# Kernel optimization log

Hardware: AMD Instinct MI355X
Metric: run time of the kernel (lower is better)

## Reference

```python
import jax, jax.numpy as jnp
import numpy as np

NG, NC, FG, FC, D = 8192, 4096, 512, 256, 64
ALPHA = 0.2          # leaky_relu negative slope
NEG = -9.0e15        # mask fill value from the torch code


def _leaky(x):
    return jnp.where(x >= 0, x, ALPHA * x)


def _relation(h_src, h_dst, a, adj):
    # additive GAT score: e[i,j] = leaky(h_src[i]@a[:D] + h_dst[j]@a[D:])
    s1 = h_src @ a[:D]            # [Ns]
    s2 = h_dst @ a[D:]            # [Nd]
    e = _leaky(s1[:, None] + s2[None, :])          # [Ns, Nd]
    att = jax.nn.softmax(jnp.where(adj > 0, e, NEG), axis=1)
    return att @ h_dst            # [Ns, D]


def setup_inputs() -> dict:
    key = jax.random.key(0)
    ks = jax.random.split(key, 14)
    sc = 0.05
    return {
        "gene_x": jax.random.normal(ks[0], (NG, FG), jnp.float32),
        "cell_x": jax.random.normal(ks[1], (NC, FC), jnp.float32),
        "W_g": jax.random.normal(ks[2], (FG, D), jnp.float32) * sc,
        "W_c": jax.random.normal(ks[3], (FC, D), jnp.float32) * sc,
        "a_gg": jax.random.normal(ks[4], (2 * D,), jnp.float32) * sc,
        "a_gc": jax.random.normal(ks[5], (2 * D,), jnp.float32) * sc,
        "a_cc": jax.random.normal(ks[6], (2 * D,), jnp.float32) * sc,
        "a_cg": jax.random.normal(ks[7], (2 * D,), jnp.float32) * sc,
        "Wgate_g": jax.random.normal(ks[8], (D, 1), jnp.float32) * sc,
        "bgate_g": jnp.full((1,), -2.0, jnp.float32),
        "Wgate_c": jax.random.normal(ks[9], (D, 1), jnp.float32) * sc,
        "bgate_c": jnp.full((1,), -2.0, jnp.float32),
        "gene_adj": jax.random.randint(ks[10], (NG, NG), 0, 2, jnp.int32),
        "cell_adj": jax.random.randint(ks[11], (NC, NC), 0, 2, jnp.int32),
        "gene_cell_adj": jax.random.randint(ks[12], (NG, NC), 0, 2, jnp.int32),
    }


def reference(gene_x, cell_x, W_g, W_c, a_gg, a_gc, a_cc, a_cg,
              Wgate_g, bgate_g, Wgate_c, bgate_c,
              gene_adj, cell_adj, gene_cell_adj):
    gene_h = gene_x @ W_g                              # [NG, D]
    cell_h = cell_x @ W_c                              # [NC, D]

    gene_from_gene = _relation(gene_h, gene_h, a_gg, gene_adj)
    gene_from_cell = _relation(gene_h, cell_h, a_gc, gene_cell_adj)
    cell_from_cell = _relation(cell_h, cell_h, a_cc, cell_adj)
    cell_from_gene = _relation(cell_h, gene_h, a_cg, gene_cell_adj.T)

    gamma_g = jax.nn.sigmoid(gene_h @ Wgate_g + bgate_g)   # [NG, 1]
    gamma_c = jax.nn.sigmoid(cell_h @ Wgate_c + bgate_c)   # [NC, 1]

    gene_out = _leaky(gene_h + gene_from_gene + gamma_g * gene_from_cell)
    cell_out = _leaky(cell_h + cell_from_cell + gamma_c * cell_from_gene)
    return gene_out, cell_out
```

## Files before the change

### kernel.cpp

```cpp
#include <hip/hip_runtime.h>

#define NG 8192
#define NC 4096
#define FG 512
#define FC 256
#define ALPHA 0.2f

typedef float f32x4 __attribute__((ext_vector_type(4)));
typedef short bf16x8 __attribute__((ext_vector_type(8)));

static __device__ __forceinline__ float leakyf(float x) { return fmaxf(x, ALPHA * x); }

static __device__ __forceinline__ unsigned short f2bf(float f) {
    unsigned u = __builtin_bit_cast(unsigned, f);
    u += 0x7fffu + ((u >> 16) & 1u);
    return (unsigned short)(u >> 16);
}

static __device__ __forceinline__ float wred(float v) {
#pragma unroll
    for (int m = 1; m < 64; m <<= 1) v += __shfl_xor(v, m, 64);
    return v;
}

__global__ __launch_bounds__(256) void proj_kernel(
    const float* __restrict__ x, const float* __restrict__ W, int K, int N,
    float* __restrict__ h, unsigned short* __restrict__ hT,
    const float* __restrict__ aA, const float* __restrict__ aB,
    const float* __restrict__ aC, const float* __restrict__ aD,
    const float* __restrict__ aG, const float* __restrict__ bG,
    float* __restrict__ sA, float* __restrict__ sB, float* __restrict__ sC,
    float* __restrict__ sD, float* __restrict__ gam)
{
    const int wave = threadIdx.x >> 6, lane = threadIdx.x & 63;
    const int r0 = blockIdx.x * 16 + wave * 4;
    const float* xr = x + (size_t)r0 * K;
    float acc0 = 0.f, acc1 = 0.f, acc2 = 0.f, acc3 = 0.f;
    for (int k = 0; k < K; k += 4) {
        float4 x0 = *(const float4*)(xr + k);
        float4 x1 = *(const float4*)(xr + K + k);
        float4 x2 = *(const float4*)(xr + 2 * (size_t)K + k);
        float4 x3 = *(const float4*)(xr + 3 * (size_t)K + k);
        float w0 = W[(k + 0) * 64 + lane];
        float w1 = W[(k + 1) * 64 + lane];
        float w2 = W[(k + 2) * 64 + lane];
        float w3 = W[(k + 3) * 64 + lane];
        acc0 += x0.x * w0 + x0.y * w1 + x0.z * w2 + x0.w * w3;
        acc1 += x1.x * w0 + x1.y * w1 + x1.z * w2 + x1.w * w3;
        acc2 += x2.x * w0 + x2.y * w1 + x2.z * w2 + x2.w * w3;
        acc3 += x3.x * w0 + x3.y * w1 + x3.z * w2 + x3.w * w3;
    }
    float accs[4] = {acc0, acc1, acc2, acc3};
    unsigned short hb[4];
#pragma unroll
    for (int t = 0; t < 4; t++) {
        h[(size_t)(r0 + t) * 64 + lane] = accs[t];
        hb[t] = f2bf(accs[t]);
    }
    *(ushort4*)&hT[(size_t)lane * N + r0] = make_ushort4(hb[0], hb[1], hb[2], hb[3]);

    const float cA = aA[lane], cB = aB[lane], cC = aC[lane], cD = aD[lane], cG = aG[lane];
    const float bias = bG[0];
#pragma unroll
    for (int t = 0; t < 4; t++) {
        float vA = wred(accs[t] * cA);
        float vB = wred(accs[t] * cB);
        float vC = wred(accs[t] * cC);
        float vD = wred(accs[t] * cD);
        float vG = wred(accs[t] * cG);
        if (lane == 0) {
            sA[r0 + t] = vA; sB[r0 + t] = vB; sC[r0 + t] = vC; sD[r0 + t] = vD;
            gam[r0 + t] = 1.f / (1.f + __expf(-(vG + bias)));
        }
    }
}

__global__ __launch_bounds__(256, 4) void rel_kernel(
    const int* __restrict__ adj, int adj_ld, int transposed,
    const float* __restrict__ s1, const float* __restrict__ s2,
    const unsigned short* __restrict__ hT, int Nd,
    float* __restrict__ num, float* __restrict__ lsum, int Ns, int JS)
{
    __shared__ unsigned short lds[64 * 264];
    const int wave = threadIdx.x >> 6, lane = threadIdx.x & 63;
    const int m = lane & 15, kp = lane >> 4;
    const int strip = blockIdx.x, p = blockIdx.y;
    const int jlen = Nd / JS;
    const int jbase = p * jlen;
    const int i_row = strip * 64 + wave * 16 + m;
    const float s1v = s1[i_row];
    f32x4 acc0 = {0.f, 0.f, 0.f, 0.f}, acc1 = acc0, acc2 = acc0, acc3 = acc0;
    float lacc = 0.f;

    for (int j0 = jbase; j0 < jbase + jlen; j0 += 256) {
        for (int idx = threadIdx.x; idx < 2048; idx += 256) {
            int c = idx >> 5, off = (idx & 31) * 8;
            *(int4*)&lds[c * 264 + off] = *(const int4*)&hT[(size_t)c * Nd + j0 + off];
        }
        __syncthreads();
#pragma unroll
        for (int kk = 0; kk < 8; kk++) {
            const int jg = j0 + kk * 32 + kp * 8;
            float s2v[8];
            {
                float4 sa = *(const float4*)&s2[jg];
                float4 sb = *(const float4*)&s2[jg + 4];
                s2v[0] = sa.x; s2v[1] = sa.y; s2v[2] = sa.z; s2v[3] = sa.w;
                s2v[4] = sb.x; s2v[5] = sb.y; s2v[6] = sb.z; s2v[7] = sb.w;
            }
            int am[8];
            if (!transposed) {
                const int* ar = adj + (size_t)i_row * adj_ld + jg;
                int4 a0 = *(const int4*)ar;
                int4 a1 = *(const int4*)(ar + 4);
                am[0] = a0.x; am[1] = a0.y; am[2] = a0.z; am[3] = a0.w;
                am[4] = a1.x; am[5] = a1.y; am[6] = a1.z; am[7] = a1.w;
            } else {
                const int* ac = adj + (size_t)jg * adj_ld + i_row;
#pragma unroll
                for (int t = 0; t < 8; t++) am[t] = ac[(size_t)t * adj_ld];
            }
            bf16x8 af;
#pragma unroll
            for (int t = 0; t < 8; t++) {
                float e = s1v + s2v[t];
                float w = (am[t] > 0) ? __expf(leakyf(e)) : 0.f;
                lacc += w;
                af[t] = (short)f2bf(w);
            }
            const int lb = kk * 32 + kp * 8;
            bf16x8 b0 = *(const bf16x8*)&lds[(0 * 16 + m) * 264 + lb];
            bf16x8 b1 = *(const bf16x8*)&lds[(1 * 16 + m) * 264 + lb];
            bf16x8 b2 = *(const bf16x8*)&lds[(2 * 16 + m) * 264 + lb];
            bf16x8 b3 = *(const bf16x8*)&lds[(3 * 16 + m) * 264 + lb];
            acc0 = __builtin_amdgcn_mfma_f32_16x16x32_bf16(af, b0, acc0, 0, 0, 0);
            acc1 = __builtin_amdgcn_mfma_f32_16x16x32_bf16(af, b1, acc1, 0, 0, 0);
            acc2 = __builtin_amdgcn_mfma_f32_16x16x32_bf16(af, b2, acc2, 0, 0, 0);
            acc3 = __builtin_amdgcn_mfma_f32_16x16x32_bf16(af, b3, acc3, 0, 0, 0);
        }
        __syncthreads();
    }
    const int orow0 = strip * 64 + wave * 16 + kp * 4;
#pragma unroll
    for (int r = 0; r < 4; r++) {
        size_t base = ((size_t)p * Ns + orow0 + r) * 64;
        num[base + m]      = acc0[r];
        num[base + 16 + m] = acc1[r];
        num[base + 32 + m] = acc2[r];
        num[base + 48 + m] = acc3[r];
    }
    lacc += __shfl_xor(lacc, 16, 64);
    lacc += __shfl_xor(lacc, 32, 64);
    if (kp == 0) lsum[(size_t)p * Ns + strip * 64 + wave * 16 + m] = lacc;
}

__global__ __launch_bounds__(256) void combine_final(
    const float* __restrict__ numS, const float* __restrict__ lS, int JSS,
    const float* __restrict__ numX, const float* __restrict__ lX, int JSX,
    int Ns, const float* __restrict__ h, const float* __restrict__ gam,
    float* __restrict__ out)
{
    int idx = blockIdx.x * 256 + threadIdx.x;
    int i = idx >> 6, c = idx & 63;
    float nS = 0.f, dS = 0.f, nX = 0.f, dX = 0.f;
    for (int p = 0; p < JSS; p++) {
        nS += numS[((size_t)p * Ns + i) * 64 + c];
        dS += lS[(size_t)p * Ns + i];
    }
    for (int p = 0; p < JSX; p++) {
        nX += numX[((size_t)p * Ns + i) * 64 + c];
        dX += lX[(size_t)p * Ns + i];
    }
    float v = h[idx] + nS / dS + gam[i] * (nX / dX);
    out[idx] = leakyf(v);
}

extern "C" void kernel_launch(void* const* d_in, const int* in_sizes, int n_in,
                              void* d_out, int out_size, void* d_ws, size_t ws_size,
                              hipStream_t stream)
{
    const float* gene_x = (const float*)d_in[0];
    const float* cell_x = (const float*)d_in[1];
    const float* W_g    = (const float*)d_in[2];
    const float* W_c    = (const float*)d_in[3];
    const float* a_gg   = (const float*)d_in[4];
    const float* a_gc   = (const float*)d_in[5];
    const float* a_cc   = (const float*)d_in[6];
    const float* a_cg   = (const float*)d_in[7];
    const float* Wgg    = (const float*)d_in[8];
    const float* bgg    = (const float*)d_in[9];
    const float* Wgc    = (const float*)d_in[10];
    const float* bgc    = (const float*)d_in[11];
    const int* gene_adj = (const int*)d_in[12];
    const int* cell_adj = (const int*)d_in[13];
    const int* gc_adj   = (const int*)d_in[14];

    size_t off = 0;
    char* wsb = (char*)d_ws;
    auto alloc = [&](size_t bytes) -> void* {
        void* p = wsb + off;
        off += (bytes + 255) & ~(size_t)255;
        return p;
    };
    const int JS = 16;
    float* gene_h = (float*)alloc((size_t)NG * 64 * 4);
    float* cell_h = (float*)alloc((size_t)NC * 64 * 4);
    unsigned short* gene_hT = (unsigned short*)alloc((size_t)NG * 64 * 2);
    unsigned short* cell_hT = (unsigned short*)alloc((size_t)NC * 64 * 2);
    float* s1gg = (float*)alloc(NG * 4);
    float* s2gg = (float*)alloc(NG * 4);
    float* s1gc = (float*)alloc(NG * 4);
    float* s2cg = (float*)alloc(NG * 4);
    float* gamg = (float*)alloc(NG * 4);
    float* s1cc = (float*)alloc(NC * 4);
    float* s2cc = (float*)alloc(NC * 4);
    float* s2gc = (float*)alloc(NC * 4);
    float* s1cg = (float*)alloc(NC * 4);
    float* gamc = (float*)alloc(NC * 4);
    float* numGG = (float*)alloc((size_t)NG * 64 * JS * 4);
    float* lGG   = (float*)alloc((size_t)NG * JS * 4);
    float* numGC = (float*)alloc((size_t)NG * 64 * JS * 4);
    float* lGC   = (float*)alloc((size_t)NG * JS * 4);
    float* numCC = (float*)alloc((size_t)NC * 64 * JS * 4);
    float* lCC   = (float*)alloc((size_t)NC * JS * 4);
    float* numCG = (float*)alloc((size_t)NC * 64 * JS * 4);
    float* lCG   = (float*)alloc((size_t)NC * JS * 4);

    float* out_gene = (float*)d_out;
    float* out_cell = (float*)d_out + (size_t)NG * 64;

    proj_kernel<<<NG / 16, 256, 0, stream>>>(gene_x, W_g, FG, NG, gene_h, gene_hT,
        a_gg, a_gg + 64, a_gc, a_cg + 64, Wgg, bgg, s1gg, s2gg, s1gc, s2cg, gamg);
    proj_kernel<<<NC / 16, 256, 0, stream>>>(cell_x, W_c, FC, NC, cell_h, cell_hT,
        a_cc, a_cc + 64, a_gc + 64, a_cg, Wgc, bgc, s1cc, s2cc, s2gc, s1cg, gamc);

    rel_kernel<<<dim3(NG / 64, JS), 256, 0, stream>>>(gene_adj, NG, 0, s1gg, s2gg,
        gene_hT, NG, numGG, lGG, NG, JS);
    rel_kernel<<<dim3(NC / 64, JS), 256, 0, stream>>>(cell_adj, NC, 0, s1cc, s2cc,
        cell_hT, NC, numCC, lCC, NC, JS);
    rel_kernel<<<dim3(NG / 64, JS), 256, 0, stream>>>(gc_adj, NC, 0, s1gc, s2gc,
        cell_hT, NC, numGC, lGC, NG, JS);
    rel_kernel<<<dim3(NC / 64, JS), 256, 0, stream>>>(gc_adj, NC, 1, s1cg, s2cg,
        gene_hT, NG, numCG, lCG, NC, JS);

    combine_final<<<NG * 64 / 256, 256, 0, stream>>>(numGG, lGG, JS, numGC, lGC, JS,
        NG, gene_h, gamg, out_gene);
    combine_final<<<NC * 64 / 256, 256, 0, stream>>>(numCC, lCC, JS, numCG, lCG, JS,
        NC, cell_h, gamc, out_cell);
}
```

Measured before the change: 729.4 us.

## Load B operand directly from global memory and retune split factors per relation

Drops the LDS staging of the transposed bf16 features and the block-wide barriers. Each lane now reads its MFMA B fragments straight from global memory, relying on cache hits, and the loop runs over 32-column groups with unroll 2. The column-split factor is cut to 8 for the gene-row relations, which halves partial-sum traffic for those relations but gives fewer blocks. The risk is more redundant global and L2 reads, since the four waves now each fetch the same B data.

```diff
diff --git a/kernel.cpp b/kernel.cpp
--- a/kernel.cpp
+++ b/kernel.cpp
@@ -81,64 +81,56 @@
     const unsigned short* __restrict__ hT, int Nd,
     float* __restrict__ num, float* __restrict__ lsum, int Ns, int JS)
 {
-    __shared__ unsigned short lds[64 * 264];
     const int wave = threadIdx.x >> 6, lane = threadIdx.x & 63;
     const int m = lane & 15, kp = lane >> 4;
     const int strip = blockIdx.x, p = blockIdx.y;
-    const int jlen = Nd / JS;
-    const int jbase = p * jlen;
+    const int jlen = Nd / JS, jbase = p * jlen;
     const int i_row = strip * 64 + wave * 16 + m;
     const float s1v = s1[i_row];
     f32x4 acc0 = {0.f, 0.f, 0.f, 0.f}, acc1 = acc0, acc2 = acc0, acc3 = acc0;
     float lacc = 0.f;
 
-    for (int j0 = jbase; j0 < jbase + jlen; j0 += 256) {
-        for (int idx = threadIdx.x; idx < 2048; idx += 256) {
-            int c = idx >> 5, off = (idx & 31) * 8;
-            *(int4*)&lds[c * 264 + off] = *(const int4*)&hT[(size_t)c * Nd + j0 + off];
+    const unsigned short* hb0 = hT + (size_t)(0 * 16 + m) * Nd;
+    const unsigned short* hb1 = hT + (size_t)(1 * 16 + m) * Nd;
+    const unsigned short* hb2 = hT + (size_t)(2 * 16 + m) * Nd;
+    const unsigned short* hb3 = hT + (size_t)(3 * 16 + m) * Nd;
+
+    const int NGRP = jlen >> 5;
+#pragma unroll 2
+    for (int g = 0; g < NGRP; ++g) {
+        const int jg = jbase + g * 32 + kp * 8;
+        float4 sa = *(const float4*)&s2[jg];
+        float4 sb = *(const float4*)&s2[jg + 4];
+        int am[8];
+        if (!transposed) {
+            const int* ar = adj + (size_t)i_row * adj_ld + jg;
+            int4 a0 = *(const int4*)ar;
+            int4 a1 = *(const int4*)(ar + 4);
+            am[0] = a0.x; am[1] = a0.y; am[2] = a0.z; am[3] = a0.w;
+            am[4] = a1.x; am[5] = a1.y; am[6] = a1.z; am[7] = a1.w;
+        } else {
+            const int* ac = adj + (size_t)jg * adj_ld + i_row;
+#pragma unroll
+            for (int t = 0; t < 8; t++) am[t] = ac[(size_t)t * adj_ld];
         }
-        __syncthreads();
-#pragma unroll
-        for (int kk = 0; kk < 8; kk++) {
-            const int jg = j0 + kk * 32 + kp * 8;
-            float s2v[8];
-            {
-                float4 sa = *(const float4*)&s2[jg];
-                float4 sb = *(const float4*)&s2[jg + 4];
-                s2v[0] = sa.x; s2v[1] = sa.y; s2v[2] = sa.z; s2v[3] = sa.w;
-                s2v[4] = sb.x; s2v[5] = sb.y; s2v[6] = sb.z; s2v[7] = sb.w;
-            }
-            int am[8];
-            if (!transposed) {
-                const int* ar = adj + (size_t)i_row * adj_ld + jg;
-                int4 a0 = *(const int4*)ar;
-                int4 a1 = *(const int4*)(ar + 4);
-                am[0] = a0.x; am[1] = a0.y; am[2] = a0.z; am[3] = a0.w;
-                am[4] = a1.x; am[5] = a1.y; am[6] = a1.z; am[7] = a1.w;
-            } else {
-                const int* ac = adj + (size_t)jg * adj_ld + i_row;
-#pragma unroll
-                for (int t = 0; t < 8; t++) am[t] = ac[(size_t)t * adj_ld];
-            }
-            bf16x8 af;
-#pragma unroll
-            for (int t = 0; t < 8; t++) {
-                float e = s1v + s2v[t];
-                float w = (am[t] > 0) ? __expf(leakyf(e)) : 0.f;
-                lacc += w;
-                af[t] = (short)f2bf(w);
-            }
-            const int lb = kk * 32 + kp * 8;
-            bf16x8 b0 = *(const bf16x8*)&lds[(0 * 16 + m) * 264 + lb];
-            bf16x8 b1 = *(const bf16x8*)&lds[(1 * 16 + m) * 264 + lb];
-            bf16x8 b2 = *(const bf16x8*)&lds[(2 * 16 + m) * 264 + lb];
-            bf16x8 b3 = *(const bf16x8*)&lds[(3 * 16 + m) * 264 + lb];
-            acc0 = __builtin_amdgcn_mfma_f32_16x16x32_bf16(af, b0, acc0, 0, 0, 0);
-            acc1 = __builtin_amdgcn_mfma_f32_16x16x32_bf16(af, b1, acc1, 0, 0, 0);
-            acc2 = __builtin_amdgcn_mfma_f32_16x16x32_bf16(af, b2, acc2, 0, 0, 0);
-            acc3 = __builtin_amdgcn_mfma_f32_16x16x32_bf16(af, b3, acc3, 0, 0, 0);
+        bf16x8 b0 = *(const bf16x8*)&hb0[jg];
+        bf16x8 b1 = *(const bf16x8*)&hb1[jg];
+        bf16x8 b2 = *(const bf16x8*)&hb2[jg];
+        bf16x8 b3 = *(const bf16x8*)&hb3[jg];
+
+        float s2v[8] = {sa.x, sa.y, sa.z, sa.w, sb.x, sb.y, sb.z, sb.w};
+        bf16x8 af;
+#pragma unroll
+        for (int t = 0; t < 8; t++) {
+            float e = s1v + s2v[t];
+            float w = (am[t] > 0) ? __expf(leakyf(e)) : 0.f;
+            lacc += w;
+            af[t] = (short)f2bf(w);
         }
-        __syncthreads();
+        acc0 = __builtin_amdgcn_mfma_f32_16x16x32_bf16(af, b0, acc0, 0, 0, 0);
+        acc1 = __builtin_amdgcn_mfma_f32_16x16x32_bf16(af, b1, acc1, 0, 0, 0);
+        acc2 = __builtin_amdgcn_mfma_f32_16x16x32_bf16(af, b2, acc2, 0, 0, 0);
+        acc3 = __builtin_amdgcn_mfma_f32_16x16x32_bf16(af, b3, acc3, 0, 0, 0);
     }
     const int orow0 = strip * 64 + wave * 16 + kp * 4;
 #pragma unroll
@@ -202,7 +194,8 @@
         off += (bytes + 255) & ~(size_t)255;
         return p;
     };
-    const int JS = 16;
+    const int JS_GG = 8, JS_CC = 16, JS_GC = 8, JS_CG = 16;
+
     float* gene_h = (float*)alloc((size_t)NG * 64 * 4);
     float* cell_h = (float*)alloc((size_t)NC * 64 * 4);
     unsigned short* gene_hT = (unsigned short*)alloc((size_t)NG * 64 * 2);
@@ -217,14 +210,14 @@
     float* s2gc = (float*)alloc(NC * 4);
     float* s1cg = (float*)alloc(NC * 4);
     float* gamc = (float*)alloc(NC * 4);
-    float* numGG = (float*)alloc((size_t)NG * 64 * JS * 4);
-    float* lGG   = (float*)alloc((size_t)NG * JS * 4);
-    float* numGC = (float*)alloc((size_t)NG * 64 * JS * 4);
-    float* lGC   = (float*)alloc((size_t)NG * JS * 4);
-    float* numCC = (float*)alloc((size_t)NC * 64 * JS * 4);
-    float* lCC   = (float*)alloc((size_t)NC * JS * 4);
-    float* numCG = (float*)alloc((size_t)NC * 64 * JS * 4);
-    float* lCG   = (float*)alloc((size_t)NC * JS * 4);
+    float* numGG = (float*)alloc((size_t)NG * 64 * JS_GG * 4);
+    float* lGG   = (float*)alloc((size_t)NG * JS_GG * 4);
+    float* numGC = (float*)alloc((size_t)NG * 64 * JS_GC * 4);
+    float* lGC   = (float*)alloc((size_t)NG * JS_GC * 4);
+    float* numCC = (float*)alloc((size_t)NC * 64 * JS_CC * 4);
+    float* lCC   = (float*)alloc((size_t)NC * JS_CC * 4);
+    float* numCG = (float*)alloc((size_t)NC * 64 * JS_CG * 4);
+    float* lCG   = (float*)alloc((size_t)NC * JS_CG * 4);
 
     float* out_gene = (float*)d_out;
     float* out_cell = (float*)d_out + (size_t)NG * 64;
@@ -234,17 +227,17 @@
     proj_kernel<<<NC / 16, 256, 0, stream>>>(cell_x, W_c, FC, NC, cell_h, cell_hT,
         a_cc, a_cc + 64, a_gc + 64, a_cg, Wgc, bgc, s1cc, s2cc, s2gc, s1cg, gamc);
 
-    rel_kernel<<<dim3(NG / 64, JS), 256, 0, stream>>>(gene_adj, NG, 0, s1gg, s2gg,
-        gene_hT, NG, numGG, lGG, NG, JS);
-    rel_kernel<<<dim3(NC / 64, JS), 256, 0, stream>>>(cell_adj, NC, 0, s1cc, s2cc,
-        cell_hT, NC, numCC, lCC, NC, JS);
-    rel_kernel<<<dim3(NG / 64, JS), 256, 0, stream>>>(gc_adj, NC, 0, s1gc, s2gc,
-        cell_hT, NC, numGC, lGC, NG, JS);
-    rel_kernel<<<dim3(NC / 64, JS), 256, 0, stream>>>(gc_adj, NC, 1, s1cg, s2cg,
-        gene_hT, NG, numCG, lCG, NC, JS);
-
-    combine_final<<<NG * 64 / 256, 256, 0, stream>>>(numGG, lGG, JS, numGC, lGC, JS,
+    rel_kernel<<<dim3(NG / 64, JS_GG), 256, 0, stream>>>(gene_adj, NG, 0, s1gg, s2gg,
+        gene_hT, NG, numGG, lGG, NG, JS_GG);
+    rel_kernel<<<dim3(NC / 64, JS_CC), 256, 0, stream>>>(cell_adj, NC, 0, s1cc, s2cc,
+        cell_hT, NC, numCC, lCC, NC, JS_CC);
+    rel_kernel<<<dim3(NG / 64, JS_GC), 256, 0, stream>>>(gc_adj, NC, 0, s1gc, s2gc,
+        cell_hT, NC, numGC, lGC, NG, JS_GC);
+    rel_kernel<<<dim3(NC / 64, JS_CG), 256, 0, stream>>>(gc_adj, NC, 1, s1cg, s2cg,
+        gene_hT, NG, numCG, lCG, NC, JS_CG);
+
+    combine_final<<<NG * 64 / 256, 256, 0, stream>>>(numGG, lGG, JS_GG, numGC, lGC, JS_GC,
         NG, gene_h, gamg, out_gene);
-    combine_final<<<NC * 64 / 256, 256, 0, stream>>>(numCC, lCC, JS, numCG, lCG, JS,
+    combine_final<<<NC * 64 / 256, 256, 0, stream>>>(numCC, lCC, JS_CC, numCG, lCG, JS_CG,
         NC, cell_h, gamc, out_cell);
 }
```

Measured after the change: 763.0 us. 1.05x slower.
